# Performance work log

Hardware: AMD Instinct MI355X
Metric: run time of the kernel (lower is better)

## Reference

```python
import jax, jax.numpy as jnp
import numpy as np

IOU_THRESHOLD = 0.7


def _pairwise_iou(boxes):
    # boxes: [N, 4] as (y1, x1, y2, x2). Returns [N, N] IoU matrix.
    y1, x1, y2, x2 = boxes[:, 0], boxes[:, 1], boxes[:, 2], boxes[:, 3]
    area = (y2 - y1) * (x2 - x1)  # [N]
    iy1 = jnp.maximum(y1[:, None], y1[None, :])
    ix1 = jnp.maximum(x1[:, None], x1[None, :])
    iy2 = jnp.minimum(y2[:, None], y2[None, :])
    ix2 = jnp.minimum(x2[:, None], x2[None, :])
    ih = jnp.clip(iy2 - iy1, 0.0)
    iw = jnp.clip(ix2 - ix1, 0.0)
    inter = ih * iw
    union = area[:, None] + area[None, :] - inter
    return inter / jnp.maximum(union, 1e-9)


def setup_inputs() -> dict:
    key = jax.random.key(0)
    k1, k2, k3 = jax.random.split(key, 3)
    n = 8192
    img = 1024.0
    # Valid boxes: top-left corner + positive width/height, clipped to image.
    tl = jax.random.uniform(k1, (n, 2), dtype=jnp.float32) * (img - 64.0)
    wh = 16.0 + jax.random.uniform(k2, (n, 2), dtype=jnp.float32) * 192.0
    br = jnp.minimum(tl + wh, img)
    bounding_box = jnp.concatenate([tl, br], axis=1)  # (y1, x1, y2, x2)
    cls_score = jax.random.uniform(k3, (n,), dtype=jnp.float32)
    return {"bounding_box": bounding_box, "cls_score": cls_score}


def reference(bounding_box, cls_score):
    # Sort by score descending.
    idx = jnp.argsort(-cls_score)
    bbox = bounding_box[idx]  # [N, 4]
    # NOTE: the original module suppresses box j if ANY earlier box i (i < j)
    # in score order overlaps it (even if box i was itself suppressed), so
    # there is no sequential dependence and it vectorizes exactly:
    iou = _pairwise_iou(bbox)  # [N, N]
    suppress = jnp.triu(iou > IOU_THRESHOLD, k=1)  # row i suppresses col j, i<j
    keep = ~jnp.any(suppress, axis=0)  # [N] bool
    # Original returns bbox[keep] (dynamic shape); for jit-compatibility we
    # return the sorted boxes with suppressed rows zeroed, plus equal math.
    return bbox * keep[:, None].astype(bbox.dtype)
```

## Files before the change

### kernel.cpp

```cpp
#include <hip/hip_runtime.h>
#include <stdint.h>

#define NBOX 8192


__global__ __launch_bounds__(256) void nms_rank_kernel(
    const float4* __restrict__ bbox, const float* __restrict__ score,
    float4* __restrict__ sbox, uint32_t* __restrict__ flags)
{
    __shared__ uint64_t keys[NBOX];
    const int t = threadIdx.x;
    if (blockIdx.x == 0) flags[t] = 0;

    #pragma unroll
    for (int s = 0; s < NBOX / 256; ++s) {
        int i = t + s * 256;
        uint32_t b = __float_as_uint(score[i]);
        keys[i] = ((uint64_t)(b ^ 0xFFFFFFFFu) << 32) | (uint32_t)i;
    }
    __syncthreads();

    const int e = blockIdx.x * 16 + (t >> 4);
    const int p = t & 15;
    const uint64_t myk = keys[e];
    int cnt = 0;
    #pragma unroll 8
    for (int s = 0; s < NBOX / 16; ++s)
        cnt += (keys[s * 16 + p] < myk) ? 1 : 0;

    cnt += __shfl_down(cnt, 8, 16);
    cnt += __shfl_down(cnt, 4, 16);
    cnt += __shfl_down(cnt, 2, 16);
    cnt += __shfl_down(cnt, 1, 16);

    if (p == 0) sbox[cnt] = bbox[e];
}

__global__ __launch_bounds__(256) void nms_suppress_kernel(
    const float4* __restrict__ sbox, uint32_t* __restrict__ flags)
{
    const int w    = (int)(threadIdx.x >> 6);
    const int lane = (int)(threadIdx.x & 63);
    const int is   = (int)(blockIdx.x >> 8);
    const int jg   = ((int)(blockIdx.x & 255)) * 4 + w;
    const int j0   = jg * 8;
    const int s0   = is * 512;
    if (s0 >= j0 + 7) return;

    int nfull = (j0 - s0) >> 6;
    if (nfull > 8) nfull = 8;
    const int pc = nfull;
    const bool partial = (pc < 8) && (s0 + pc * 64 < j0 + 7);

    float jy1[8], jx1[8], jy2[8], jx2[8], ja[8], tk[8];
    #pragma unroll
    for (int k = 0; k < 8; ++k) {
        float4 b = sbox[j0 + k];
        jy1[k] = b.x; jx1[k] = b.y; jy2[k] = b.z; jx2[k] = b.w;
        ja[k] = (b.z - b.x) * (b.w - b.y);
        tk[k] = 0.4110f * ja[k];
    }

    uint32_t hit = 0;
    float4 cur = sbox[s0 + lane];

    for (int c = 0; c < nfull; ++c) {
        float4 nxt = sbox[s0 + (c + 1) * 64 + lane];

        const float iy1 = cur.x, ix1 = cur.y, iy2 = cur.z, ix2 = cur.w;
        const float ia  = (iy2 - iy1) * (ix2 - ix1);
        const float tia = 0.4110f * ia;

        int cand = 0;
        #pragma unroll
        for (int k = 0; k < 8; ++k) {
            float ty1 = fmaxf(iy1, jy1[k]);
            float tx1 = fmaxf(ix1, jx1[k]);
            float ty2 = fminf(iy2, jy2[k]);
            float tx2 = fminf(ix2, jx2[k]);
            float ih = fmaxf(ty2 - ty1, 0.0f);
            float iw = fmaxf(tx2 - tx1, 0.0f);
            float inter = ih * iw;
            cand |= __any(inter > tia + tk[k]);
        }
        if (cand) {
            #pragma unroll
            for (int k = 0; k < 8; ++k) {
                float ty1 = fmaxf(iy1, jy1[k]);
                float tx1 = fmaxf(ix1, jx1[k]);
                float ty2 = fminf(iy2, jy2[k]);
                float tx2 = fminf(ix2, jx2[k]);
                float ih = fmaxf(ty2 - ty1, 0.0f);
                float iw = fmaxf(tx2 - tx1, 0.0f);
                float inter = ih * iw;
                float s  = ia + ja[k];
                float un = s - inter;
                float iou = inter / fmaxf(un, 1e-9f);
                if (iou > 0.7f) hit |= (1u << k);
            }
        }
        cur = nxt;
    }

    if (partial) {
        const int i = s0 + pc * 64 + lane;
        const float iy1 = cur.x, ix1 = cur.y, iy2 = cur.z, ix2 = cur.w;
        const float ia  = (iy2 - iy1) * (ix2 - ix1);
        const float tia = 0.4110f * ia;

        int cand = 0;
        #pragma unroll
        for (int k = 0; k < 8; ++k) {
            float ty1 = fmaxf(iy1, jy1[k]);
            float tx1 = fmaxf(ix1, jx1[k]);
            float ty2 = fminf(iy2, jy2[k]);
            float tx2 = fminf(ix2, jx2[k]);
            float ih = fmaxf(ty2 - ty1, 0.0f);
            float iw = fmaxf(tx2 - tx1, 0.0f);
            float inter = ih * iw;
            cand |= __any((i < j0 + k) & (inter > tia + tk[k]));
        }
        if (cand) {
            #pragma unroll
            for (int k = 0; k < 8; ++k) {
                float ty1 = fmaxf(iy1, jy1[k]);
                float tx1 = fmaxf(ix1, jx1[k]);
                float ty2 = fminf(iy2, jy2[k]);
                float tx2 = fminf(ix2, jx2[k]);
                float ih = fmaxf(ty2 - ty1, 0.0f);
                float iw = fmaxf(tx2 - tx1, 0.0f);
                float inter = ih * iw;
                float s  = ia + ja[k];
                float un = s - inter;
                float iou = inter / fmaxf(un, 1e-9f);
                if ((i < j0 + k) & (iou > 0.7f)) hit |= (1u << k);
            }
        }
    }

    uint32_t byte = 0;
    #pragma unroll
    for (int k = 0; k < 8; ++k)
        if (__any(hit & (1u << k))) byte |= (1u << k);
    if (lane == 0 && byte)
        atomicOr(&flags[jg >> 2], byte << ((jg & 3) * 8));
}

__global__ __launch_bounds__(256) void nms_write_kernel(
    const float4* __restrict__ sbox, const uint32_t* __restrict__ flags,
    float4* __restrict__ out)
{
    int j = blockIdx.x * 256 + threadIdx.x;
    bool sup = (flags[j >> 5] >> (j & 31)) & 1u;
    float4 v = sbox[j];
    if (sup) { v.x = 0.0f; v.y = 0.0f; v.z = 0.0f; v.w = 0.0f; }
    out[j] = v;
}

extern "C" void kernel_launch(void* const* d_in, const int* in_sizes, int n_in,
                              void* d_out, int out_size, void* d_ws, size_t ws_size,
                              hipStream_t stream) {
    const float4* bbox  = (const float4*)d_in[0];
    const float*  score = (const float*)d_in[1];
    float4* out = (float4*)d_out;
    float4* sbox = (float4*)d_ws;
    uint32_t* flags = (uint32_t*)((float*)d_ws + 4 * NBOX);

    hipLaunchKernelGGL(nms_rank_kernel, dim3(NBOX / 16), dim3(256), 0, stream,
                       bbox, score, sbox, flags);
    hipLaunchKernelGGL(nms_suppress_kernel, dim3(4096), dim3(256), 0, stream,
                       sbox, flags);
    hipLaunchKernelGGL(nms_write_kernel, dim3(NBOX / 256), dim3(256), 0, stream,
                       sbox, flags, out);
}
```

Baseline: 36.99 us.

## Compact suppress grid to triangular tiles and shrink rank keys to 32-bit

The suppress kernel now maps each wave to a valid (i-stripe, j-group) pair in the lower triangle, so the grid drops from 4096 blocks (many exiting early) to 2176 live blocks. It also adds a two-deep prefetch of the box stream and raises the occupancy hint. The rank kernel stores 32-bit raw score bits in shared memory instead of 64-bit keys, loads them with vector copies, and breaks ties by index explicitly. This halves LDS traffic, but the unsigned compare on raw float bits assumes scores are non-negative. The per-wave loop that decodes the triangular index adds a small serial cost.

Result: slower. 41.62 us (+12.5%).

```diff
diff --git a/kernel.cpp b/kernel.cpp
--- a/kernel.cpp
+++ b/kernel.cpp
@@ -5,29 +5,31 @@
 
 
 __global__ __launch_bounds__(256) void nms_rank_kernel(
-    const float4* __restrict__ bbox, const float* __restrict__ score,
+    const float4* __restrict__ bbox, const uint32_t* __restrict__ scoreBits,
     float4* __restrict__ sbox, uint32_t* __restrict__ flags)
 {
-    __shared__ uint64_t keys[NBOX];
+    __shared__ uint32_t keys[NBOX];
     const int t = threadIdx.x;
     if (blockIdx.x == 0) flags[t] = 0;
 
     #pragma unroll
-    for (int s = 0; s < NBOX / 256; ++s) {
-        int i = t + s * 256;
-        uint32_t b = __float_as_uint(score[i]);
-        keys[i] = ((uint64_t)(b ^ 0xFFFFFFFFu) << 32) | (uint32_t)i;
-    }
+    for (int s = 0; s < NBOX / 1024; ++s)
+        ((uint4*)keys)[t + s * 256] = ((const uint4*)scoreBits)[t + s * 256];
     __syncthreads();
 
     const int e = blockIdx.x * 16 + (t >> 4);
     const int p = t & 15;
-    const uint64_t myk = keys[e];
+    const uint32_t m = keys[e];
     int cnt = 0;
-    #pragma unroll 8
-    for (int s = 0; s < NBOX / 16; ++s)
-        cnt += (keys[s * 16 + p] < myk) ? 1 : 0;
-
+    #pragma unroll 4
+    for (int s = 0; s < NBOX / 64; ++s) {
+        uint4 kb = ((const uint4*)keys)[s * 16 + p];
+        int ib = s * 64 + p * 4;
+        cnt += (int)(kb.x > m) + (int)((kb.x == m) & (ib + 0 < e));
+        cnt += (int)(kb.y > m) + (int)((kb.y == m) & (ib + 1 < e));
+        cnt += (int)(kb.z > m) + (int)((kb.z == m) & (ib + 2 < e));
+        cnt += (int)(kb.w > m) + (int)((kb.w == m) & (ib + 3 < e));
+    }
     cnt += __shfl_down(cnt, 8, 16);
     cnt += __shfl_down(cnt, 4, 16);
     cnt += __shfl_down(cnt, 2, 16);
@@ -36,16 +38,17 @@
     if (p == 0) sbox[cnt] = bbox[e];
 }
 
-__global__ __launch_bounds__(256) void nms_suppress_kernel(
+__global__ __launch_bounds__(256, 4) void nms_suppress_kernel(
     const float4* __restrict__ sbox, uint32_t* __restrict__ flags)
 {
-    const int w    = (int)(threadIdx.x >> 6);
     const int lane = (int)(threadIdx.x & 63);
-    const int is   = (int)(blockIdx.x >> 8);
-    const int jg   = ((int)(blockIdx.x & 255)) * 4 + w;
-    const int j0   = jg * 8;
-    const int s0   = is * 512;
-    if (s0 >= j0 + 7) return;
+    const int w    = (int)(blockIdx.x * 4 + (threadIdx.x >> 6));
+
+    int is = 0, rem = w;
+    while (rem >= 1024 - 64 * is) { rem -= 1024 - 64 * is; ++is; }
+    const int jg = 1023 - rem;
+    const int j0 = jg * 8;
+    const int s0 = is * 512;
 
     int nfull = (j0 - s0) >> 6;
     if (nfull > 8) nfull = 8;
@@ -62,16 +65,18 @@
     }
 
     uint32_t hit = 0;
-    float4 cur = sbox[s0 + lane];
+    float4 A = sbox[s0 + lane];
+    float4 B = sbox[s0 + (pc > 0 ? 64 : 0) + lane];
 
     for (int c = 0; c < nfull; ++c) {
-        float4 nxt = sbox[s0 + (c + 1) * 64 + lane];
+        int nidx = c + 2; if (nidx > pc) nidx = pc;
+        float4 N = sbox[s0 + nidx * 64 + lane];
 
-        const float iy1 = cur.x, ix1 = cur.y, iy2 = cur.z, ix2 = cur.w;
+        const float iy1 = A.x, ix1 = A.y, iy2 = A.z, ix2 = A.w;
         const float ia  = (iy2 - iy1) * (ix2 - ix1);
         const float tia = 0.4110f * ia;
 
-        int cand = 0;
+        unsigned long long candm = 0;
         #pragma unroll
         for (int k = 0; k < 8; ++k) {
             float ty1 = fmaxf(iy1, jy1[k]);
@@ -81,9 +86,9 @@
             float ih = fmaxf(ty2 - ty1, 0.0f);
             float iw = fmaxf(tx2 - tx1, 0.0f);
             float inter = ih * iw;
-            cand |= __any(inter > tia + tk[k]);
+            candm |= __ballot(inter > tia + tk[k]);
         }
-        if (cand) {
+        if (candm) {
             #pragma unroll
             for (int k = 0; k < 8; ++k) {
                 float ty1 = fmaxf(iy1, jy1[k]);
@@ -99,16 +104,16 @@
                 if (iou > 0.7f) hit |= (1u << k);
             }
         }
-        cur = nxt;
+        A = B; B = N;
     }
 
     if (partial) {
         const int i = s0 + pc * 64 + lane;
-        const float iy1 = cur.x, ix1 = cur.y, iy2 = cur.z, ix2 = cur.w;
+        const float iy1 = A.x, ix1 = A.y, iy2 = A.z, ix2 = A.w;
         const float ia  = (iy2 - iy1) * (ix2 - ix1);
         const float tia = 0.4110f * ia;
 
-        int cand = 0;
+        unsigned long long candm = 0;
         #pragma unroll
         for (int k = 0; k < 8; ++k) {
             float ty1 = fmaxf(iy1, jy1[k]);
@@ -118,9 +123,9 @@
             float ih = fmaxf(ty2 - ty1, 0.0f);
             float iw = fmaxf(tx2 - tx1, 0.0f);
             float inter = ih * iw;
-            cand |= __any((i < j0 + k) & (inter > tia + tk[k]));
+            candm |= __ballot((i < j0 + k) & (inter > tia + tk[k]));
         }
-        if (cand) {
+        if (candm) {
             #pragma unroll
             for (int k = 0; k < 8; ++k) {
                 float ty1 = fmaxf(iy1, jy1[k]);
@@ -160,15 +165,15 @@
 extern "C" void kernel_launch(void* const* d_in, const int* in_sizes, int n_in,
                               void* d_out, int out_size, void* d_ws, size_t ws_size,
                               hipStream_t stream) {
-    const float4* bbox  = (const float4*)d_in[0];
-    const float*  score = (const float*)d_in[1];
+    const float4*   bbox  = (const float4*)d_in[0];
+    const uint32_t* sbits = (const uint32_t*)d_in[1];
     float4* out = (float4*)d_out;
     float4* sbox = (float4*)d_ws;
     uint32_t* flags = (uint32_t*)((float*)d_ws + 4 * NBOX);
 
     hipLaunchKernelGGL(nms_rank_kernel, dim3(NBOX / 16), dim3(256), 0, stream,
-                       bbox, score, sbox, flags);
-    hipLaunchKernelGGL(nms_suppress_kernel, dim3(4096), dim3(256), 0, stream,
+                       bbox, sbits, sbox, flags);
+    hipLaunchKernelGGL(nms_suppress_kernel, dim3(2176), dim3(256), 0, stream,
                        sbox, flags);
     hipLaunchKernelGGL(nms_write_kernel, dim3(NBOX / 256), dim3(256), 0, stream,
                        sbox, flags, out);
```

## Add shared-memory n-body suppression kernel over triangular block tiles

Applied to the files above, without the earlier changes.

Adds a second suppression kernel that maps blocks onto a triangular tiling of the i<j pairs. Each block stages 128 preceding boxes in shared memory and each thread tests one box j, using a double-precision exact IoU threshold comparison in place of a division. The old suppression kernel is still launched first, so the new kernel adds work on top of it rather than replacing it. It also clamps nfull at zero and rewrites the flags pointer arithmetic without changing its value.

Measured after the change: 58.85 us. +59.1%, slower.

```diff
diff --git a/kernel.cpp b/kernel.cpp
--- a/kernel.cpp
+++ b/kernel.cpp
@@ -48,6 +48,7 @@
     if (s0 >= j0 + 7) return;
 
     int nfull = (j0 - s0) >> 6;
+    if (nfull < 0) nfull = 0;
     if (nfull > 8) nfull = 8;
     const int pc = nfull;
     const bool partial = (pc < 8) && (s0 + pc * 64 < j0 + 7);
@@ -146,6 +147,63 @@
         atomicOr(&flags[jg >> 2], byte << ((jg & 3) * 8));
 }
 
+__device__ __forceinline__ bool iou_hit(float4 bi, float ia,
+                                        float jy1, float jx1, float jy2,
+                                        float jx2, float ja) {
+    const double MD = (double)0.7f + 0x1.0p-25;
+    float ty1 = fmaxf(bi.x, jy1);
+    float tx1 = fmaxf(bi.y, jx1);
+    float ty2 = fminf(bi.z, jy2);
+    float tx2 = fminf(bi.w, jx2);
+    float ih = fmaxf(__fsub_rn(ty2, ty1), 0.0f);
+    float iw = fmaxf(__fsub_rn(tx2, tx1), 0.0f);
+    float inter = __fmul_rn(ih, iw);
+    float s  = __fadd_rn(ia, ja);
+    float un = __fsub_rn(s, inter);
+    return (double)inter >= MD * (double)un;
+}
+
+__global__ __launch_bounds__(256, 4) void nms_suppress_nbody(
+    const float4* __restrict__ sbox, uint32_t* __restrict__ flags)
+{
+    __shared__ float4 LB[128];
+    __shared__ float  LA[128];
+    const int tid = threadIdx.x;
+    const int b = (int)blockIdx.x;
+
+    int jb = (int)((sqrtf(4.0f * (float)b + 1.0f) - 1.0f) * 0.5f);
+    while ((jb + 1) * (jb + 2) <= b) ++jb;
+    while (jb * (jb + 1) > b) --jb;
+    const int t = b - jb * (jb + 1);
+    const int ibase = t * 128;
+    const int j = jb * 256 + tid;
+
+    if (tid < 128) {
+        float4 bx = sbox[ibase + tid];
+        LB[tid] = bx;
+        LA[tid] = __fmul_rn(__fsub_rn(bx.z, bx.x), __fsub_rn(bx.w, bx.y));
+    }
+    float4 bj = sbox[j];
+    const float jy1 = bj.x, jx1 = bj.y, jy2 = bj.z, jx2 = bj.w;
+    const float ja = __fmul_rn(__fsub_rn(bj.z, bj.x), __fsub_rn(bj.w, bj.y));
+    __syncthreads();
+
+    bool supp = false;
+    if (t < 2 * jb) {
+        #pragma unroll 4
+        for (int ii = 0; ii < 128; ++ii)
+            supp |= iou_hit(LB[ii], LA[ii], jy1, jx1, jy2, jx2, ja);
+    } else {
+        #pragma unroll 4
+        for (int ii = 0; ii < 128; ++ii) {
+            bool ok = (ibase + ii) < j;
+            supp |= ok & iou_hit(LB[ii], LA[ii], jy1, jx1, jy2, jx2, ja);
+        }
+    }
+
+    if (supp) atomicOr(&flags[j >> 5], 1u << (j & 31));
+}
+
 __global__ __launch_bounds__(256) void nms_write_kernel(
     const float4* __restrict__ sbox, const uint32_t* __restrict__ flags,
     float4* __restrict__ out)
@@ -164,12 +222,14 @@
     const float*  score = (const float*)d_in[1];
     float4* out = (float4*)d_out;
     float4* sbox = (float4*)d_ws;
-    uint32_t* flags = (uint32_t*)((float*)d_ws + 4 * NBOX);
+    uint32_t* flags = (uint32_t*)((char*)d_ws + NBOX * 16);
 
     hipLaunchKernelGGL(nms_rank_kernel, dim3(NBOX / 16), dim3(256), 0, stream,
                        bbox, score, sbox, flags);
     hipLaunchKernelGGL(nms_suppress_kernel, dim3(4096), dim3(256), 0, stream,
                        sbox, flags);
+    hipLaunchKernelGGL(nms_suppress_nbody, dim3(1056), dim3(256), 0, stream,
+                       sbox, flags);
     hipLaunchKernelGGL(nms_write_kernel, dim3(NBOX / 256), dim3(256), 0, stream,
                        sbox, flags, out);
 }
```
